# Kernel tuning notes

Hardware: AMD Instinct MI355X
Metric: run time of the kernel (lower is better)

Reference implementation:

```python
import math
import jax, jax.numpy as jnp
import numpy as np

KS = 64        # top-k kept candidates per query
INIT_W = 16    # initial grid width
NEG = -1e9     # mask fill value


def setup_inputs() -> dict:
    key0 = jax.random.key(0)
    k1, k2, k3 = jax.random.split(key0, 3)
    N, T, H = 16, 2048, 64
    return {
        "query": jax.random.normal(k1, (N, T, H), jnp.float32),
        "key": jax.random.normal(k2, (N, T, H), jnp.float32),
        "value": jax.random.normal(k3, (N, T, H), jnp.float32),
    }


def _gather(x, idx):
    # x: [N, S, H], idx: [N, T, Z] -> [N, T, Z, H]
    return jnp.take_along_axis(x[:, None, :, :], idx[..., None], axis=2)


def _tree_indices(query, key):
    """Hierarchical tree top-k refinement (approx_mask): start from INIT_W
    coarse grid cells, repeatedly split each cell (scale_up=2), score the
    representative key of each cell against the query (sampled sparse matmul),
    and keep the top-KS cells, until cell width reaches 1 token."""
    N, T, H = query.shape
    S = key.shape[1]
    # causal per-row source length: tsrcs = arange(T_SRC+1-T_DST, T_SRC+1)
    tsrc = jnp.arange(S - T + 1, S + 1, dtype=jnp.float32)[None, :, None]  # [1,T,1]

    w = INIT_W
    zs = jnp.broadcast_to(jnp.arange(INIT_W, dtype=jnp.int32)[None, None, :], (N, T, INIT_W))
    mask = jnp.ones((N, T, INIT_W), dtype=bool)

    n_iter = int(math.log2(S // INIT_W))  # fixed iteration count (static shapes)
    for _ in range(n_iter):
        w2 = w * 2
        # resize: each cell z -> children (2z, 2z+1) on the finer grid
        zs = jnp.stack([zs * 2, zs * 2 + 1], axis=-1).reshape(N, T, -1)
        mask = jnp.repeat(mask, 2, axis=-1)
        # score representative key at cell start: pos = round(z * tsrc / w)
        pos = jnp.clip(jnp.round(zs.astype(jnp.float32) * (tsrc / w2)).astype(jnp.int32), 0, S - 1)
        scores = jnp.einsum('nth,ntzh->ntz', query, _gather(key, pos))
        scores = jnp.where(mask, scores, NEG)
        # topk_prime: keep top-k cells
        K = min(KS, zs.shape[-1])
        _, top_i = jax.lax.top_k(scores, K)
        zs = jnp.take_along_axis(zs, top_i, axis=-1)
        mask = jnp.take_along_axis(mask, top_i, axis=-1)
        w = w2
    # final token positions, causal validity
    pos = jnp.clip(jnp.round(zs.astype(jnp.float32) * (tsrc / w)).astype(jnp.int32), 0, S - 1)
    mask = mask & (pos.astype(jnp.float32) < tsrc)
    return pos, mask


def reference(query, key, value):
    N, T, H = query.shape
    pos, mask = _tree_indices(query, key)            # [N,T,K] int, bool
    ksel = _gather(key, pos)                          # [N,T,K,H]
    vsel = _gather(value, pos)                        # [N,T,K,H]
    scores = jnp.einsum('nth,ntzh->ntz', query, ksel) / math.sqrt(H)
    scores = jnp.where(mask, scores, NEG)
    p = jax.nn.softmax(scores, axis=-1)
    p = jnp.where(mask, p, 0.0)
    return jnp.einsum('ntz,ntzh->nth', p, vsel)
```

## Files before the change

### kernel.cpp

```cpp
#include <hip/hip_runtime.h>
#include <math.h>


constexpr int Tn = 2048;
constexpr int Hn = 64;
constexpr int WV = 4;
constexpr float NEGF = -1e9f;

typedef unsigned long long u64;
typedef unsigned int u32;

#define WWAIT() asm volatile("s_waitcnt lgkmcnt(0)" ::: "memory")

__device__ __forceinline__ u32 ord32(float f) {
    u32 u = __float_as_uint(f);
    return (u & 0x80000000u) ? ~u : (u | 0x80000000u);
}
__device__ __forceinline__ u64 packkey(float s, int e) {
    return ((u64)ord32(s) << 32) | (u64)(u32)(~e);
}
__device__ __forceinline__ float dec_score(u64 k) {
    u32 o = (u32)(k >> 32);
    u32 u = (o & 0x80000000u) ? (o & 0x7fffffffu) : ~o;
    return __uint_as_float(u);
}
__device__ __forceinline__ int dec_e(u64 k) { return (int)(~(u32)k); }

__device__ __forceinline__ int cpos(int z, float ratio) {
    float x = (float)z * ratio;
    int p = (int)rintf(x);
    p = p < 0 ? 0 : p;
    p = p > (Tn - 1) ? (Tn - 1) : p;
    return p;
}

__device__ __forceinline__ float dotq(const float* __restrict__ krow,
                                      const float* qs) {
    float acc = 0.f;
#pragma unroll
    for (int h = 0; h < Hn; h += 4) {
        float4 kv = *reinterpret_cast<const float4*>(krow + h);
        float4 qv = *reinterpret_cast<const float4*>(qs + h);
        acc = fmaf(qv.x, kv.x, acc);
        acc = fmaf(qv.y, kv.y, acc);
        acc = fmaf(qv.z, kv.z, acc);
        acc = fmaf(qv.w, kv.w, acc);
    }
    return acc;
}

__device__ __forceinline__ u64 shflx64(u64 v, int m) {
    u32 lo = (u32)__shfl_xor((int)(u32)v, m, 64);
    u32 hi = (u32)__shfl_xor((int)(v >> 32), m, 64);
    return ((u64)hi << 32) | lo;
}

template<int N>
__device__ __forceinline__ u64 bitonic_desc(u64 key, int lane) {
#pragma unroll
    for (int k = 2; k <= N; k <<= 1) {
#pragma unroll
        for (int j = k >> 1; j >= 1; j >>= 1) {
            u64 pk = shflx64(key, j);
            bool wmax = (((lane & j) == 0) == ((lane & k) == 0));
            key = ((key > pk) == wmax) ? key : pk;
        }
    }
    return key;
}

template<int N>
__device__ __forceinline__ int cnt_gt(const u64* D, u64 x) {
    int c = 0;
#pragma unroll
    for (int s = N; s >= 1; s >>= 1) {
        if (c + s <= N && D[c + s - 1] > x) c += s;
    }
    return c;
}

__global__ void __launch_bounds__(256)
TreeAttention_70257075028607_kernel(
        const float* __restrict__ Q, const float* __restrict__ Kk,
        const float* __restrict__ V, float* __restrict__ O) {
    __shared__ __align__(16) float qsh[WV][Hn];
    __shared__ __align__(16) u64   Lsh[WV][64];
    __shared__ __align__(16) u64   Rsh[WV][64];
    __shared__ __align__(16) u64   Osh[WV][64];

    const int lane = threadIdx.x & 63;
    const int wv   = threadIdx.x >> 6;
    const int row  = blockIdx.x * WV + wv;
    const int n    = row >> 11;
    const int t    = row & (Tn - 1);
    const float tp1 = (float)(t + 1);

    const float* qrow = Q + (size_t)row * Hn;
    const float* Kb   = Kk + (size_t)n * Tn * Hn;
    const float* Vb   = V  + (size_t)n * Tn * Hn;

    float* qs = qsh[wv];
    u64* Lb = Lsh[wv];
    u64* Rb = Rsh[wv];
    u64* Ob = Osh[wv];

    qs[lane] = qrow[lane];
    WWAIT();

    int   myz  = 0;
    float mysc = NEGF;

    {
        const float ratio = tp1 * (1.f / 32.f);
        u64 key;
        if (lane < 32) {
            float s = dotq(Kb + (size_t)cpos(lane, ratio) * Hn, qs);
            key = packkey(s, lane);
        } else {
            key = (u64)lane;
        }
        key = bitonic_desc<32>(key, lane);
        if (lane < 32) { myz = dec_e(key); mysc = dec_score(key); }
    }

    {
        const float ratio = tp1 * (1.f / 64.f);
        u64 Lk = packkey(mysc, 2 * lane);
        u64 Rs;
        if (lane < 32) {
            float s1 = dotq(Kb + (size_t)cpos(2 * myz + 1, ratio) * Hn, qs);
            Rs = packkey(s1, 2 * lane + 1);
        } else {
            Rs = (u64)lane;
        }
        Rs = bitonic_desc<32>(Rs, lane);
        if (lane < 32) { Lb[lane] = Lk; Rb[lane] = Rs; }
        WWAIT();
        if (lane < 32) {
            int rL = lane + cnt_gt<32>(Rb, Lk);
            int rR = lane + cnt_gt<32>(Lb, Rs);
            Ob[rL] = Lk;
            Ob[rR] = Rs;
        }
        WWAIT();
        u64 kk = Ob[lane];
        int e  = dec_e(kk);
        int pz = __shfl(myz, e >> 1, 64);
        myz  = 2 * pz + (e & 1);
        mysc = dec_score(kk);
    }

#pragma unroll
    for (int it = 0; it < 5; ++it) {
        const float ratio = tp1 * ldexpf(1.0f, -(7 + it));
        float s1 = dotq(Kb + (size_t)cpos(2 * myz + 1, ratio) * Hn, qs);
        u64 Lk = packkey(mysc, 2 * lane);
        u64 Rs = bitonic_desc<64>(packkey(s1, 2 * lane + 1), lane);
        Lb[lane] = Lk;
        Rb[lane] = Rs;
        WWAIT();
        int rL = lane + cnt_gt<64>(Rb, Lk);
        int rR = lane + cnt_gt<64>(Lb, Rs);
        if (rL < 64) Ob[rL] = Lk;
        if (rR < 64) Ob[rR] = Rs;
        WWAIT();
        u64 kk = Ob[lane];
        int e  = dec_e(kk);
        int pz = __shfl(myz, e >> 1, 64);
        myz  = 2 * pz + (e & 1);
        mysc = dec_score(kk);
    }

    {
        int mypos  = cpos(myz, tp1 * (1.f / 2048.f));
        bool valid = ((float)mypos < tp1);
        float s = valid ? mysc * 0.125f : NEGF;

        float m = s;
#pragma unroll
        for (int off = 32; off >= 1; off >>= 1)
            m = fmaxf(m, __shfl_xor(m, off, 64));
        float p = expf(s - m);
        float sum = p;
#pragma unroll
        for (int off = 32; off >= 1; off >>= 1)
            sum += __shfl_xor(sum, off, 64);
        p = p / sum;
        if (!valid) p = 0.f;

        Ob[lane] = ((u64)(u32)mypos << 32) | __float_as_uint(p);
        WWAIT();

        float acc = 0.f;
#pragma unroll 8
        for (int jj = 0; jj < 64; ++jj) {
            u64 w = Ob[jj];
            acc = fmaf(__uint_as_float((u32)w),
                       Vb[(size_t)(w >> 32) * Hn + lane], acc);
        }
        O[(size_t)row * Hn + lane] = acc;
    }
}

extern "C" void kernel_launch(void* const* d_in, const int* in_sizes, int n_in,
                              void* d_out, int out_size, void* d_ws, size_t ws_size,
                              hipStream_t stream) {
    const float* Q = (const float*)d_in[0];
    const float* K = (const float*)d_in[1];
    const float* V = (const float*)d_in[2];
    float* O = (float*)d_out;

    const int rows = in_sizes[0] / Hn;
    const int blocks = rows / WV;
    TreeAttention_70257075028607_kernel<<<blocks, WV * 64, 0, stream>>>(Q, K, V, O);
}
```

Baseline: 439.9 us.

## Stage gathered key rows through LDS with async global_load_lds double buffering

```diff
diff --git a/kernel.cpp b/kernel.cpp
--- a/kernel.cpp
+++ b/kernel.cpp
@@ -11,6 +11,7 @@
 typedef unsigned int u32;
 
 #define WWAIT() asm volatile("s_waitcnt lgkmcnt(0)" ::: "memory")
+#define VMW(n)  asm volatile("s_waitcnt vmcnt(" #n ")" ::: "memory")
 
 __device__ __forceinline__ u32 ord32(float f) {
     u32 u = __float_as_uint(f);
@@ -34,21 +35,6 @@
     return p;
 }
 
-__device__ __forceinline__ float dotq(const float* __restrict__ krow,
-                                      const float* qs) {
-    float acc = 0.f;
-#pragma unroll
-    for (int h = 0; h < Hn; h += 4) {
-        float4 kv = *reinterpret_cast<const float4*>(krow + h);
-        float4 qv = *reinterpret_cast<const float4*>(qs + h);
-        acc = fmaf(qv.x, kv.x, acc);
-        acc = fmaf(qv.y, kv.y, acc);
-        acc = fmaf(qv.z, kv.z, acc);
-        acc = fmaf(qv.w, kv.w, acc);
-    }
-    return acc;
-}
-
 __device__ __forceinline__ u64 shflx64(u64 v, int m) {
     u32 lo = (u32)__shfl_xor((int)(u32)v, m, 64);
     u32 hi = (u32)__shfl_xor((int)(v >> 32), m, 64);
@@ -79,11 +65,75 @@
     return c;
 }
 
+typedef const __attribute__((address_space(1))) unsigned int gas_u32;
+typedef __attribute__((address_space(3))) unsigned int las_u32;
+__device__ __forceinline__ void gll16(const float* g, float* l) {
+    __builtin_amdgcn_global_load_lds((gas_u32*)g, (las_u32*)l, 16, 0, 0);
+}
+
+template<int R>
+__device__ __forceinline__ void stage_chunk(const float* __restrict__ Kb,
+                                            int posme, int c, float* buf,
+                                            int lane) {
+#pragma unroll
+    for (int k = 0; k < R / 16; ++k) {
+        int r = 16 * k + (lane >> 2);
+        int p = __shfl(posme, r, 64);
+        int piece = (lane & 3) ^ ((r >> 1) & 3);
+        const float* src = Kb + (size_t)p * Hn + c * 16 + piece * 4;
+        gll16(src, buf + k * 256);
+    }
+}
+
+__device__ __forceinline__ float dot_chunk(const float* buf, const float* qs,
+                                           int c, int lane, float acc) {
+    const int swz = (lane >> 1) & 3;
+    const float4* row = reinterpret_cast<const float4*>(buf + lane * 16);
+    float4 v0 = row[0 ^ swz];
+    float4 v1 = row[1 ^ swz];
+    float4 v2 = row[2 ^ swz];
+    float4 v3 = row[3 ^ swz];
+    const float4* qv = reinterpret_cast<const float4*>(qs + c * 16);
+    float4 q0 = qv[0], q1 = qv[1], q2 = qv[2], q3 = qv[3];
+    acc = fmaf(q0.x, v0.x, acc); acc = fmaf(q0.y, v0.y, acc);
+    acc = fmaf(q0.z, v0.z, acc); acc = fmaf(q0.w, v0.w, acc);
+    acc = fmaf(q1.x, v1.x, acc); acc = fmaf(q1.y, v1.y, acc);
+    acc = fmaf(q1.z, v1.z, acc); acc = fmaf(q1.w, v1.w, acc);
+    acc = fmaf(q2.x, v2.x, acc); acc = fmaf(q2.y, v2.y, acc);
+    acc = fmaf(q2.z, v2.z, acc); acc = fmaf(q2.w, v2.w, acc);
+    acc = fmaf(q3.x, v3.x, acc); acc = fmaf(q3.y, v3.y, acc);
+    acc = fmaf(q3.z, v3.z, acc); acc = fmaf(q3.w, v3.w, acc);
+    return acc;
+}
+
+template<int R>
+__device__ __forceinline__ float scored(const float* __restrict__ Kb,
+                                        const float* qs, float* bufA,
+                                        float* bufB, int posme, int lane) {
+    stage_chunk<R>(Kb, posme, 0, bufA, lane);
+    stage_chunk<R>(Kb, posme, 1, bufB, lane);
+    float acc = 0.f;
+    if constexpr (R == 64) { VMW(4); } else { VMW(2); }
+    acc = dot_chunk(bufA, qs, 0, lane, acc);
+    WWAIT();
+    stage_chunk<R>(Kb, posme, 2, bufA, lane);
+    if constexpr (R == 64) { VMW(4); } else { VMW(2); }
+    acc = dot_chunk(bufB, qs, 1, lane, acc);
+    WWAIT();
+    stage_chunk<R>(Kb, posme, 3, bufB, lane);
+    if constexpr (R == 64) { VMW(4); } else { VMW(2); }
+    acc = dot_chunk(bufA, qs, 2, lane, acc);
+    VMW(0);
+    acc = dot_chunk(bufB, qs, 3, lane, acc);
+    return acc;
+}
+
 __global__ void __launch_bounds__(256)
 TreeAttention_70257075028607_kernel(
         const float* __restrict__ Q, const float* __restrict__ Kk,
         const float* __restrict__ V, float* __restrict__ O) {
     __shared__ __align__(16) float qsh[WV][Hn];
+    __shared__ __align__(16) float kbsh[WV][2][1024];
     __shared__ __align__(16) u64   Lsh[WV][64];
     __shared__ __align__(16) u64   Rsh[WV][64];
     __shared__ __align__(16) u64   Osh[WV][64];
@@ -99,7 +149,9 @@
     const float* Kb   = Kk + (size_t)n * Tn * Hn;
     const float* Vb   = V  + (size_t)n * Tn * Hn;
 
-    float* qs = qsh[wv];
+    float* qs  = qsh[wv];
+    float* kbA = kbsh[wv][0];
+    float* kbB = kbsh[wv][1];
     u64* Lb = Lsh[wv];
     u64* Rb = Rsh[wv];
     u64* Ob = Osh[wv];
@@ -112,27 +164,19 @@
 
     {
         const float ratio = tp1 * (1.f / 32.f);
-        u64 key;
-        if (lane < 32) {
-            float s = dotq(Kb + (size_t)cpos(lane, ratio) * Hn, qs);
-            key = packkey(s, lane);
-        } else {
-            key = (u64)lane;
-        }
+        int posme = cpos(lane, ratio);
+        float s = scored<32>(Kb, qs, kbA, kbB, posme, lane);
+        u64 key = (lane < 32) ? packkey(s, lane) : (u64)lane;
         key = bitonic_desc<32>(key, lane);
         if (lane < 32) { myz = dec_e(key); mysc = dec_score(key); }
     }
 
     {
         const float ratio = tp1 * (1.f / 64.f);
+        int posme = cpos(2 * myz + 1, ratio);
+        float s1 = scored<32>(Kb, qs, kbA, kbB, posme, lane);
         u64 Lk = packkey(mysc, 2 * lane);
-        u64 Rs;
-        if (lane < 32) {
-            float s1 = dotq(Kb + (size_t)cpos(2 * myz + 1, ratio) * Hn, qs);
-            Rs = packkey(s1, 2 * lane + 1);
-        } else {
-            Rs = (u64)lane;
-        }
+        u64 Rs = (lane < 32) ? packkey(s1, 2 * lane + 1) : (u64)lane;
         Rs = bitonic_desc<32>(Rs, lane);
         if (lane < 32) { Lb[lane] = Lk; Rb[lane] = Rs; }
         WWAIT();
@@ -153,7 +197,8 @@
 #pragma unroll
     for (int it = 0; it < 5; ++it) {
         const float ratio = tp1 * ldexpf(1.0f, -(7 + it));
-        float s1 = dotq(Kb + (size_t)cpos(2 * myz + 1, ratio) * Hn, qs);
+        int posme = cpos(2 * myz + 1, ratio);
+        float s1 = scored<64>(Kb, qs, kbA, kbB, posme, lane);
         u64 Lk = packkey(mysc, 2 * lane);
         u64 Rs = bitonic_desc<64>(packkey(s1, 2 * lane + 1), lane);
         Lb[lane] = Lk;
```

Result: faster. 406.8 us (-7.5%).

## Use shuffles for merge rank search and float4 gathers for value accumulation

Applied to the files above, without the earlier changes.

```diff
diff --git a/kernel.cpp b/kernel.cpp
--- a/kernel.cpp
+++ b/kernel.cpp
@@ -54,6 +54,11 @@
     u32 hi = (u32)__shfl_xor((int)(v >> 32), m, 64);
     return ((u64)hi << 32) | lo;
 }
+__device__ __forceinline__ u64 shflv64(u64 v, int idx) {
+    u32 lo = (u32)__shfl((int)(u32)v, idx, 64);
+    u32 hi = (u32)__shfl((int)(v >> 32), idx, 64);
+    return ((u64)hi << 32) | lo;
+}
 
 template<int N>
 __device__ __forceinline__ u64 bitonic_desc(u64 key, int lane) {
@@ -70,11 +75,13 @@
 }
 
 template<int N>
-__device__ __forceinline__ int cnt_gt(const u64* D, u64 x) {
+__device__ __forceinline__ int cntgt(u64 dist, u64 x) {
     int c = 0;
 #pragma unroll
     for (int s = N; s >= 1; s >>= 1) {
-        if (c + s <= N && D[c + s - 1] > x) c += s;
+        int idx = c + s - 1;
+        u64 pr = shflv64(dist, idx & 63);
+        if (idx < N && pr > x) c += s;
     }
     return c;
 }
@@ -84,8 +91,6 @@
         const float* __restrict__ Q, const float* __restrict__ Kk,
         const float* __restrict__ V, float* __restrict__ O) {
     __shared__ __align__(16) float qsh[WV][Hn];
-    __shared__ __align__(16) u64   Lsh[WV][64];
-    __shared__ __align__(16) u64   Rsh[WV][64];
     __shared__ __align__(16) u64   Osh[WV][64];
 
     const int lane = threadIdx.x & 63;
@@ -100,8 +105,6 @@
     const float* Vb   = V  + (size_t)n * Tn * Hn;
 
     float* qs = qsh[wv];
-    u64* Lb = Lsh[wv];
-    u64* Rb = Rsh[wv];
     u64* Ob = Osh[wv];
 
     qs[lane] = qrow[lane];
@@ -134,11 +137,9 @@
             Rs = (u64)lane;
         }
         Rs = bitonic_desc<32>(Rs, lane);
-        if (lane < 32) { Lb[lane] = Lk; Rb[lane] = Rs; }
-        WWAIT();
+        int rL = lane + cntgt<32>(Rs, Lk);
+        int rR = lane + cntgt<32>(Lk, Rs);
         if (lane < 32) {
-            int rL = lane + cnt_gt<32>(Rb, Lk);
-            int rR = lane + cnt_gt<32>(Lb, Rs);
             Ob[rL] = Lk;
             Ob[rR] = Rs;
         }
@@ -156,11 +157,8 @@
         float s1 = dotq(Kb + (size_t)cpos(2 * myz + 1, ratio) * Hn, qs);
         u64 Lk = packkey(mysc, 2 * lane);
         u64 Rs = bitonic_desc<64>(packkey(s1, 2 * lane + 1), lane);
-        Lb[lane] = Lk;
-        Rb[lane] = Rs;
-        WWAIT();
-        int rL = lane + cnt_gt<64>(Rb, Lk);
-        int rR = lane + cnt_gt<64>(Lb, Rs);
+        int rL = lane + cntgt<64>(Rs, Lk);
+        int rR = lane + cntgt<64>(Lk, Rs);
         if (rL < 64) Ob[rL] = Lk;
         if (rR < 64) Ob[rR] = Rs;
         WWAIT();
@@ -191,14 +189,30 @@
         Ob[lane] = ((u64)(u32)mypos << 32) | __float_as_uint(p);
         WWAIT();
 
-        float acc = 0.f;
-#pragma unroll 8
-        for (int jj = 0; jj < 64; ++jj) {
-            u64 w = Ob[jj];
-            acc = fmaf(__uint_as_float((u32)w),
-                       Vb[(size_t)(w >> 32) * Hn + lane], acc);
-        }
-        O[(size_t)row * Hn + lane] = acc;
+        const int seg = lane & 15;
+        const int cls = lane >> 4;
+        float ax = 0.f, ay = 0.f, az = 0.f, aw = 0.f;
+#pragma unroll
+        for (int i = 0; i < 16; ++i) {
+            u64 w = Ob[i * 4 + cls];
+            float pj = __uint_as_float((u32)w);
+            const float4 v = *reinterpret_cast<const float4*>(
+                Vb + (size_t)(w >> 32) * Hn + seg * 4);
+            ax = fmaf(pj, v.x, ax);
+            ay = fmaf(pj, v.y, ay);
+            az = fmaf(pj, v.z, az);
+            aw = fmaf(pj, v.w, aw);
+        }
+        ax += __shfl_xor(ax, 16, 64); ay += __shfl_xor(ay, 16, 64);
+        az += __shfl_xor(az, 16, 64); aw += __shfl_xor(aw, 16, 64);
+        ax += __shfl_xor(ax, 32, 64); ay += __shfl_xor(ay, 32, 64);
+        az += __shfl_xor(az, 32, 64); aw += __shfl_xor(aw, 32, 64);
+
+        if (lane < 16) {
+            float4 o4;
+            o4.x = ax; o4.y = ay; o4.z = az; o4.w = aw;
+            *reinterpret_cast<float4*>(O + (size_t)row * Hn + lane * 4) = o4;
+        }
     }
 }
 
```

New measurement: 468.5 us. 1.06x slower.
